# Kernel optimization log

Hardware: AMD Instinct MI355X
Metric: run time of the kernel (lower is better)

## Reference

```python
import jax, jax.numpy as jnp
import numpy as np

B = 65536

def setup_inputs() -> dict:
    key = jax.random.key(0)
    k1, k2 = jax.random.split(key, 2)
    x = jax.random.normal(k1, (B, 1, 28, 28), dtype=jnp.float32)
    # classifier params: Linear(4*14*14 -> 10)
    W = jax.random.normal(k2, (10, 4 * 14 * 14), dtype=jnp.float32) * 0.03
    b = jnp.zeros((10,), dtype=jnp.float32)
    return {"x": x, "W": W, "b": b}


def reference(x, W, b):
    # x: [B,1,28,28]
    batch = x.shape[0]
    img = x[:, 0]  # [B,28,28]
    # non-overlapping 2x2 patches, row-major over (r,c), flattened row-major
    # within patch -> matches torch's x[:, r:r+2, c:c+2].view(B, -1)
    patches = img.reshape(batch, 14, 2, 14, 2).transpose(0, 1, 3, 2, 4)
    patches = patches.reshape(batch, 196, 4)
    # Exact closed form of the 4-qubit circuit RY(theta_i) on wire i followed
    # by CNOT chain (0->1->2->3) and <Z_k> measurement:
    #   <Z_k> = prod_{j<=k} cos(theta_j)
    ez = jnp.cumprod(jnp.cos(patches), axis=-1)  # [B,196,4]
    feat = ez.reshape(batch, 4 * 14 * 14)  # [B,784]
    logits = feat @ W.T + b  # [B,10]
    return jax.nn.log_softmax(logits, axis=-1)
```

## Files before the change

kernel.cpp:

```cpp
#include <hip/hip_runtime.h>

#define NCLS 10
#define IMG_PIX 784
#define NUM_IMG 65536

__global__ __launch_bounds__(448, 7) void quanv_logits_kernel(
    const float* __restrict__ x,
    const float* __restrict__ W,
    const float* __restrict__ bias,
    float* __restrict__ out)
{
    __shared__ float part[64][73];

    const int tid  = threadIdx.x;
    const int wv   = __builtin_amdgcn_readfirstlane(tid >> 6);
    const int lane = tid & 63;
    const int img  = (blockIdx.x << 6) + lane;
    const float* __restrict__ p = x + (size_t)img * IMG_PIX;

    float acc[NCLS];
#pragma unroll
    for (int c = 0; c < NCLS; ++c) acc[c] = 0.0f;

#pragma unroll
    for (int rr = 0; rr < 2; ++rr) {
        const int r = wv + rr * 7;
        float rowt[28], rowb[28];
        const float4* rt = reinterpret_cast<const float4*>(p + r * 56);
        const float4* rb = reinterpret_cast<const float4*>(p + r * 56 + 28);
#pragma unroll
        for (int q = 0; q < 7; ++q) {
            float4 t  = rt[q];
            float4 bm = rb[q];
            rowt[4*q+0] = t.x;  rowt[4*q+1] = t.y;  rowt[4*q+2] = t.z;  rowt[4*q+3] = t.w;
            rowb[4*q+0] = bm.x; rowb[4*q+1] = bm.y; rowb[4*q+2] = bm.z; rowb[4*q+3] = bm.w;
        }
        const int rowbase = r * 14;
#pragma unroll
        for (int j = 0; j < 14; ++j) {
            float e0 = __cosf(rowt[2*j]);
            float e1 = e0 * __cosf(rowt[2*j + 1]);
            float e2 = e1 * __cosf(rowb[2*j]);
            float e3 = e2 * __cosf(rowb[2*j + 1]);
            const int base = (rowbase + j) * 4;
#pragma unroll
            for (int c = 0; c < NCLS; ++c) {
                float4 wq = *reinterpret_cast<const float4*>(W + c * IMG_PIX + base);
                acc[c] = fmaf(e0, wq.x, acc[c]);
                acc[c] = fmaf(e1, wq.y, acc[c]);
                acc[c] = fmaf(e2, wq.z, acc[c]);
                acc[c] = fmaf(e3, wq.w, acc[c]);
            }
        }
    }

#pragma unroll
    for (int c = 0; c < NCLS; ++c) part[lane][wv * NCLS + c] = acc[c];
    __syncthreads();

    if (wv == 0) {
        float s[NCLS];
#pragma unroll
        for (int c = 0; c < NCLS; ++c) s[c] = bias[c];
        for (int ww = 0; ww < 7; ++ww) {
#pragma unroll
            for (int c = 0; c < NCLS; ++c) s[c] += part[lane][ww * NCLS + c];
        }
        float m = s[0];
#pragma unroll
        for (int c = 1; c < NCLS; ++c) m = fmaxf(m, s[c]);
        float sum = 0.0f;
#pragma unroll
        for (int c = 0; c < NCLS; ++c) sum += __expf(s[c] - m);
        const float lse = __logf(sum) + m;

        float* o = out + (size_t)img * NCLS;
#pragma unroll
        for (int c = 0; c < NCLS; c += 2) {
            float2 v;
            v.x = s[c]     - lse;
            v.y = s[c + 1] - lse;
            *reinterpret_cast<float2*>(o + c) = v;
        }
    }
}

extern "C" void kernel_launch(void* const* d_in, const int* in_sizes, int n_in,
                              void* d_out, int out_size, void* d_ws, size_t ws_size,
                              hipStream_t stream) {
    const float* x    = (const float*)d_in[0];
    const float* W    = (const float*)d_in[1];
    const float* bias = (const float*)d_in[2];
    float* out        = (float*)d_out;

    dim3 block(448);
    dim3 grid(NUM_IMG / 64);
    quanv_logits_kernel<<<grid, block, 0, stream>>>(x, W, bias, out);
}
```

Baseline: 320.1 us.

## Stage image rows into LDS with async global_load_lds double buffering

Each wave no longer loads two full 28-pixel row pairs per lane into registers. All 7 waves now cooperatively stream one patch-row (56 floats per image) at a time into LDS, using global_load_lds 16-byte async copies into a double buffer. Each wave then handles two patches of the current row. The aim is fewer registers and overlap of the global loads with cos/FMA compute. The cost is 14 block-wide barriers per block, more LDS traffic, and reliance on the LDS-direct load builtin's layout semantics.

```diff
diff --git a/kernel.cpp b/kernel.cpp
--- a/kernel.cpp
+++ b/kernel.cpp
@@ -1,8 +1,14 @@
 #include <hip/hip_runtime.h>
 
 #define NCLS 10
-#define IMG_PIX 784
 #define NUM_IMG 65536
+
+__device__ __forceinline__ void async_cp16(const float* g, float* l) {
+    __builtin_amdgcn_global_load_lds(
+        (const __attribute__((address_space(1))) void*)(g),
+        (__attribute__((address_space(3))) void*)(l),
+        16, 0, 0);
+}
 
 __global__ __launch_bounds__(448, 7) void quanv_logits_kernel(
     const float* __restrict__ x,
@@ -10,61 +16,72 @@
     const float* __restrict__ bias,
     float* __restrict__ out)
 {
-    __shared__ float part[64][73];
+    __shared__ float sb[2 * 14 * 256];
 
     const int tid  = threadIdx.x;
-    const int wv   = __builtin_amdgcn_readfirstlane(tid >> 6);
+    const int w    = __builtin_amdgcn_readfirstlane(tid >> 6);
     const int lane = tid & 63;
-    const int img  = (blockIdx.x << 6) + lane;
-    const float* __restrict__ p = x + (size_t)img * IMG_PIX;
+    const int img0 = blockIdx.x << 6;
+    const float* __restrict__ xg = x + (size_t)(img0 + lane) * 784;
 
     float acc[NCLS];
 #pragma unroll
     for (int c = 0; c < NCLS; ++c) acc[c] = 0.0f;
 
+    const int k0 = 2 * w, k1 = 2 * w + 1;
+
+    async_cp16(xg + k0 * 4, &sb[k0 * 256]);
+    async_cp16(xg + k1 * 4, &sb[k1 * 256]);
+    __syncthreads();
+
 #pragma unroll
-    for (int rr = 0; rr < 2; ++rr) {
-        const int r = wv + rr * 7;
-        float rowt[28], rowb[28];
-        const float4* rt = reinterpret_cast<const float4*>(p + r * 56);
-        const float4* rb = reinterpret_cast<const float4*>(p + r * 56 + 28);
+    for (int rr = 0; rr < 14; ++rr) {
+        const int cur = rr & 1, nxt = cur ^ 1;
+        if (rr < 13) {
+            const float* g = xg + (rr + 1) * 56;
+            async_cp16(g + k0 * 4, &sb[(nxt * 14 + k0) * 256]);
+            async_cp16(g + k1 * 4, &sb[(nxt * 14 + k1) * 256]);
+        }
+
+        const float4 t4 = *reinterpret_cast<const float4*>(&sb[(cur * 14 + w) * 256 + lane * 4]);
+        const float4 b4 = *reinterpret_cast<const float4*>(&sb[(cur * 14 + w + 7) * 256 + lane * 4]);
+
+        const float e0 = __cosf(t4.x);
+        const float e1 = e0 * __cosf(t4.y);
+        const float e2 = e1 * __cosf(b4.x);
+        const float e3 = e2 * __cosf(b4.y);
+        const float f0 = __cosf(t4.z);
+        const float f1 = f0 * __cosf(t4.w);
+        const float f2 = f1 * __cosf(b4.z);
+        const float f3 = f2 * __cosf(b4.w);
+
+        const int P = (rr * 14 + 2 * w) * 4;
 #pragma unroll
-        for (int q = 0; q < 7; ++q) {
-            float4 t  = rt[q];
-            float4 bm = rb[q];
-            rowt[4*q+0] = t.x;  rowt[4*q+1] = t.y;  rowt[4*q+2] = t.z;  rowt[4*q+3] = t.w;
-            rowb[4*q+0] = bm.x; rowb[4*q+1] = bm.y; rowb[4*q+2] = bm.z; rowb[4*q+3] = bm.w;
+        for (int c = 0; c < NCLS; ++c) {
+            const float4 wa = *reinterpret_cast<const float4*>(&W[c * 784 + P]);
+            const float4 wb = *reinterpret_cast<const float4*>(&W[c * 784 + P + 4]);
+            float a = acc[c];
+            a = fmaf(e0, wa.x, a); a = fmaf(e1, wa.y, a);
+            a = fmaf(e2, wa.z, a); a = fmaf(e3, wa.w, a);
+            a = fmaf(f0, wb.x, a); a = fmaf(f1, wb.y, a);
+            a = fmaf(f2, wb.z, a); a = fmaf(f3, wb.w, a);
+            acc[c] = a;
         }
-        const int rowbase = r * 14;
-#pragma unroll
-        for (int j = 0; j < 14; ++j) {
-            float e0 = __cosf(rowt[2*j]);
-            float e1 = e0 * __cosf(rowt[2*j + 1]);
-            float e2 = e1 * __cosf(rowb[2*j]);
-            float e3 = e2 * __cosf(rowb[2*j + 1]);
-            const int base = (rowbase + j) * 4;
-#pragma unroll
-            for (int c = 0; c < NCLS; ++c) {
-                float4 wq = *reinterpret_cast<const float4*>(W + c * IMG_PIX + base);
-                acc[c] = fmaf(e0, wq.x, acc[c]);
-                acc[c] = fmaf(e1, wq.y, acc[c]);
-                acc[c] = fmaf(e2, wq.z, acc[c]);
-                acc[c] = fmaf(e3, wq.w, acc[c]);
-            }
-        }
+        __syncthreads();
     }
 
+    float* part = sb;
 #pragma unroll
-    for (int c = 0; c < NCLS; ++c) part[lane][wv * NCLS + c] = acc[c];
+    for (int c = 0; c < NCLS; ++c) part[lane * 71 + w * NCLS + c] = acc[c];
     __syncthreads();
 
-    if (wv == 0) {
+    if (w == 0) {
         float s[NCLS];
 #pragma unroll
         for (int c = 0; c < NCLS; ++c) s[c] = bias[c];
         for (int ww = 0; ww < 7; ++ww) {
 #pragma unroll
-            for (int c = 0; c < NCLS; ++c) s[c] += part[lane][ww * NCLS + c];
+            for (int c = 0; c < NCLS; ++c) s[c] += part[lane * 71 + ww * NCLS + c];
         }
         float m = s[0];
 #pragma unroll
@@ -74,7 +91,7 @@
         for (int c = 0; c < NCLS; ++c) sum += __expf(s[c] - m);
         const float lse = __logf(sum) + m;
 
-        float* o = out + (size_t)img * NCLS;
+        float* o = out + (size_t)(img0 + lane) * NCLS;
 #pragma unroll
         for (int c = 0; c < NCLS; c += 2) {
             float2 v;
```

Result: faster. 303.3 us (-5.2%).
